# Performance work log

Hardware: AMD Instinct MI355X
Metric: run time of the kernel (lower is better)

## Reference

```python
import jax, jax.numpy as jnp
import numpy as np
import math

VOCAB = 32000
D = 1024
SEQ = 2048
BATCH = 4
PAD_IDX = 0
LN_EPS = 1e-5


def make_sinusoidal_pe(max_len, d):
    position = jnp.arange(max_len, dtype=jnp.float32)[:, None]
    div_term = jnp.exp(jnp.arange(0, d, 2, dtype=jnp.float32) * (-math.log(10000.0) / d))
    ang = position * div_term  # [max_len, d/2]
    pe = jnp.zeros((max_len, d), dtype=jnp.float32)
    pe = pe.at[:, 0::2].set(jnp.sin(ang))
    pe = pe.at[:, 1::2].set(jnp.cos(ang))
    return pe


def verse_weights(verse_positions):
    # weight = 1.2 at the first token of each nonzero-verse run (zeros are skipped
    # and do not reset the run), else 1.0. Vectorized via forward-fill of the
    # last nonzero verse id strictly before each position.
    v = verse_positions  # [B, S] int
    S = v.shape[1]
    idx = jnp.where(v != 0, jnp.arange(S)[None, :], -1)
    last_idx = jax.lax.cummax(idx, axis=1)
    prev_idx = jnp.concatenate([jnp.full_like(last_idx[:, :1], -1), last_idx[:, :-1]], axis=1)
    prev_verse = jnp.take_along_axis(v, jnp.clip(prev_idx, 0, None), axis=1)
    prev_verse = jnp.where(prev_idx >= 0, prev_verse, -1)
    return jnp.where((v != 0) & (v != prev_verse), 1.2, 1.0).astype(jnp.float32)


def setup_inputs() -> dict:
    key = jax.random.key(0)
    k1, k2, k3, k4, k5, k6, k7 = jax.random.split(key, 7)
    token_ids = jax.random.randint(k1, (BATCH, SEQ), 0, VOCAB)
    verse_positions = jnp.sort(jax.random.randint(k2, (BATCH, SEQ), 0, 200), axis=-1)
    book_types = jax.random.randint(k3, (BATCH, SEQ), 0, 4)
    # Xavier-uniform embedding table with padding row zeroed
    limit = math.sqrt(6.0 / (VOCAB + D))
    emb_table = jax.random.uniform(k4, (VOCAB, D), jnp.float32, -limit, limit)
    emb_table = emb_table.at[PAD_IDX].set(0.0)
    book_table = jax.random.normal(k5, (4, D), jnp.float32)
    ln_gamma = jnp.ones((D,), jnp.float32)
    ln_beta = jnp.zeros((D,), jnp.float32)
    return {
        "token_ids": token_ids,
        "verse_positions": verse_positions,
        "book_types": book_types,
        "emb_table": emb_table,
        "book_table": book_table,
        "ln_gamma": ln_gamma,
        "ln_beta": ln_beta,
    }


def reference(token_ids, verse_positions, book_types, emb_table, book_table, ln_gamma, ln_beta):
    # Token embedding * sqrt(d)
    x = emb_table[token_ids] * jnp.asarray(math.sqrt(D), jnp.float32)  # [B,S,D]
    # Verse-weighted sinusoidal positional encoding (dropout = identity, eval mode)
    pe = make_sinusoidal_pe(SEQ, D)[None, :, :]  # [1,S,D]
    w = verse_weights(verse_positions)  # [B,S]
    x = x + pe * w[:, :, None]
    # Book-type embedding
    x = x + book_table[book_types]
    # LayerNorm
    mu = jnp.mean(x, axis=-1, keepdims=True)
    var = jnp.mean(jnp.square(x - mu), axis=-1, keepdims=True)
    x = (x - mu) * jax.lax.rsqrt(var + LN_EPS) * ln_gamma + ln_beta
    return x
```

## Files before the change

kernel.cpp:

```cpp
#include <hip/hip_runtime.h>

#define VOCAB 32000
#define DIM   1024
#define SEQ_  2048
#define NBAT  4

__global__ __launch_bounds__(256) void verse_embed_ln_kernel(
    const int*   __restrict__ token_ids,
    const int*   __restrict__ verse_pos,
    const int*   __restrict__ book_types,
    const float* __restrict__ emb_table,
    const float* __restrict__ book_table,
    const float* __restrict__ gamma,
    const float* __restrict__ beta,
    float*       __restrict__ out)
{
    const int wid  = threadIdx.x >> 6;
    const int lane = threadIdx.x & 63;
    const int row  = (blockIdx.x << 2) + wid;
    const int s    = row & (SEQ_ - 1);

    const int tok   = token_ids[row];
    const int bt    = book_types[row];
    const int v     = verse_pos[row];
    const int vprev = (s == 0) ? -1 : verse_pos[row - 1];
    const float w = (v != 0 && v != vprev) ? 1.2f : 1.0f;

    const float* __restrict__ erow = emb_table  + (size_t)tok * DIM;
    const float* __restrict__ brow = book_table + (size_t)bt  * DIM;

    float4 e[4], bk[4];
    #pragma unroll
    for (int c = 0; c < 4; ++c) {
        const int d0 = (c << 8) + (lane << 2);
        e[c]  = *reinterpret_cast<const float4*>(erow + d0);
        bk[c] = *reinterpret_cast<const float4*>(brow + d0);
    }

    const float C2  = -13.287712379549449f / 1024.0f;
    const float sf  = (float)s;
    const float SQD = 32.0f;

    float x[16];
    float sum = 0.0f, sq = 0.0f;
    #pragma unroll
    for (int c = 0; c < 4; ++c) {
        const int d0 = (c << 8) + (lane << 2);
        const float f0 = exp2f(C2 * (float)d0);
        const float f1 = exp2f(C2 * (float)(d0 + 2));
        float s0, c0, s1, c1;
        __sincosf(sf * f0, &s0, &c0);
        __sincosf(sf * f1, &s1, &c1);
        const float x0 = e[c].x * SQD + s0 * w + bk[c].x;
        const float x1 = e[c].y * SQD + c0 * w + bk[c].y;
        const float x2 = e[c].z * SQD + s1 * w + bk[c].z;
        const float x3 = e[c].w * SQD + c1 * w + bk[c].w;
        x[4 * c + 0] = x0; x[4 * c + 1] = x1; x[4 * c + 2] = x2; x[4 * c + 3] = x3;
        sum += (x0 + x1) + (x2 + x3);
        sq  += (x0 * x0 + x1 * x1) + (x2 * x2 + x3 * x3);
    }

    #pragma unroll
    for (int off = 32; off >= 1; off >>= 1) {
        sum += __shfl_xor(sum, off, 64);
        sq  += __shfl_xor(sq,  off, 64);
    }

    const float mean = sum * (1.0f / (float)DIM);
    const float var  = sq * (1.0f / (float)DIM) - mean * mean;
    const float rstd = rsqrtf(var + 1e-5f);

    float* __restrict__ orow = out + (size_t)row * DIM;
    #pragma unroll
    for (int c = 0; c < 4; ++c) {
        const int d0 = (c << 8) + (lane << 2);
        const float4 g  = *reinterpret_cast<const float4*>(gamma + d0);
        const float4 bb = *reinterpret_cast<const float4*>(beta  + d0);
        float4 o;
        o.x = (x[4 * c + 0] - mean) * rstd * g.x + bb.x;
        o.y = (x[4 * c + 1] - mean) * rstd * g.y + bb.y;
        o.z = (x[4 * c + 2] - mean) * rstd * g.z + bb.z;
        o.w = (x[4 * c + 3] - mean) * rstd * g.w + bb.w;
        *reinterpret_cast<float4*>(orow + d0) = o;
    }
}

extern "C" void kernel_launch(void* const* d_in, const int* in_sizes, int n_in,
                              void* d_out, int out_size, void* d_ws, size_t ws_size,
                              hipStream_t stream) {
    const int*   token_ids  = (const int*)d_in[0];
    const int*   verse_pos  = (const int*)d_in[1];
    const int*   book_types = (const int*)d_in[2];
    const float* emb_table  = (const float*)d_in[3];
    const float* book_table = (const float*)d_in[4];
    const float* ln_gamma   = (const float*)d_in[5];
    const float* ln_beta    = (const float*)d_in[6];
    float* out = (float*)d_out;

    dim3 grid((NBAT * SEQ_) / 4);
    dim3 block(256);
    verse_embed_ln_kernel<<<grid, block, 0, stream>>>(
        token_ids, verse_pos, book_types, emb_table, book_table,
        ln_gamma, ln_beta, out);
}
```

Before: 16.51 us.

## Process two rows per wave, stage book table in LDS, reuse frequency terms

Each wavefront now handles two consecutive rows, and the grid is halved. The 4-row book table is staged into shared memory once per block, and gamma/beta are loaded once per wave and reused for both rows. Per-element exp2 frequency computation is replaced by one exp2 per lane, with later frequencies derived by multiplying with constants. This cuts redundant global loads and transcendental work. In exchange it adds a block-wide sync, higher register pressure, and fewer blocks.

Result: no change. 16.49 us (-0.1%).

```diff
diff --git a/kernel.cpp b/kernel.cpp
--- a/kernel.cpp
+++ b/kernel.cpp
@@ -1,6 +1,5 @@
 #include <hip/hip_runtime.h>
 
-#define VOCAB 32000
 #define DIM   1024
 #define SEQ_  2048
 #define NBAT  4
@@ -15,73 +14,94 @@
     const float* __restrict__ beta,
     float*       __restrict__ out)
 {
-    const int wid  = threadIdx.x >> 6;
-    const int lane = threadIdx.x & 63;
-    const int row  = (blockIdx.x << 2) + wid;
-    const int s    = row & (SEQ_ - 1);
+    __shared__ float4 bookLDS[1024];
 
-    const int tok   = token_ids[row];
-    const int bt    = book_types[row];
-    const int v     = verse_pos[row];
-    const int vprev = (s == 0) ? -1 : verse_pos[row - 1];
-    const float w = (v != 0 && v != vprev) ? 1.2f : 1.0f;
+    const int t    = threadIdx.x;
+    const int wid  = t >> 6;
+    const int lane = t & 63;
+    const int base = ((blockIdx.x << 2) + wid) << 1;
 
-    const float* __restrict__ erow = emb_table  + (size_t)tok * DIM;
-    const float* __restrict__ brow = book_table + (size_t)bt  * DIM;
+    const float4* __restrict__ bt4 = reinterpret_cast<const float4*>(book_table);
+    #pragma unroll
+    for (int k = 0; k < 4; ++k)
+        bookLDS[k * 256 + t] = bt4[k * 256 + t];
 
-    float4 e[4], bk[4];
+    const int tok0 = token_ids[base],   tok1 = token_ids[base + 1];
+    const int bt0  = book_types[base],  bt1  = book_types[base + 1];
+    const int v0   = verse_pos[base],   v1   = verse_pos[base + 1];
+    const int s0   = base & (SEQ_ - 1);
+    const int vp0  = (s0 == 0) ? -1 : verse_pos[base - 1];
+    const float w0 = (v0 != 0 && v0 != vp0) ? 1.2f : 1.0f;
+    const float w1 = (v1 != 0 && v1 != v0)  ? 1.2f : 1.0f;
+
+    const float4* __restrict__ er0 = reinterpret_cast<const float4*>(emb_table) + (size_t)tok0 * 256;
+    const float4* __restrict__ er1 = reinterpret_cast<const float4*>(emb_table) + (size_t)tok1 * 256;
+    float4 e[2][4];
     #pragma unroll
-    for (int c = 0; c < 4; ++c) {
-        const int d0 = (c << 8) + (lane << 2);
-        e[c]  = *reinterpret_cast<const float4*>(erow + d0);
-        bk[c] = *reinterpret_cast<const float4*>(brow + d0);
-    }
+    for (int c = 0; c < 4; ++c) e[0][c] = er0[c * 64 + lane];
+    #pragma unroll
+    for (int c = 0; c < 4; ++c) e[1][c] = er1[c * 64 + lane];
 
-    const float C2  = -13.287712379549449f / 1024.0f;
-    const float sf  = (float)s;
+    const float4* __restrict__ g4 = reinterpret_cast<const float4*>(gamma);
+    const float4* __restrict__ b4 = reinterpret_cast<const float4*>(beta);
+    float4 g[4], b[4];
+    #pragma unroll
+    for (int c = 0; c < 4; ++c) { g[c] = g4[c * 64 + lane]; b[c] = b4[c * 64 + lane]; }
+
+    const float C2 = -13.287712379549449f / 1024.0f;
+    const float K2 = 0.9821718931198913f;
+    const int   dl = lane << 2;
+    const float fb0 = exp2f(C2 * (float)dl);
     const float SQD = 32.0f;
 
-    float x[16];
-    float sum = 0.0f, sq = 0.0f;
-    #pragma unroll
-    for (int c = 0; c < 4; ++c) {
-        const int d0 = (c << 8) + (lane << 2);
-        const float f0 = exp2f(C2 * (float)d0);
-        const float f1 = exp2f(C2 * (float)(d0 + 2));
-        float s0, c0, s1, c1;
-        __sincosf(sf * f0, &s0, &c0);
-        __sincosf(sf * f1, &s1, &c1);
-        const float x0 = e[c].x * SQD + s0 * w + bk[c].x;
-        const float x1 = e[c].y * SQD + c0 * w + bk[c].y;
-        const float x2 = e[c].z * SQD + s1 * w + bk[c].z;
-        const float x3 = e[c].w * SQD + c1 * w + bk[c].w;
-        x[4 * c + 0] = x0; x[4 * c + 1] = x1; x[4 * c + 2] = x2; x[4 * c + 3] = x3;
-        sum += (x0 + x1) + (x2 + x3);
-        sq  += (x0 * x0 + x1 * x1) + (x2 * x2 + x3 * x3);
-    }
+    __syncthreads();
 
     #pragma unroll
-    for (int off = 32; off >= 1; off >>= 1) {
-        sum += __shfl_xor(sum, off, 64);
-        sq  += __shfl_xor(sq,  off, 64);
-    }
+    for (int r = 0; r < 2; ++r) {
+        const int row = base + r;
+        const float sf = (float)(row & (SEQ_ - 1));
+        const float w  = r ? w1 : w0;
+        const int  bt  = r ? bt1 : bt0;
+        const float4* __restrict__ bkl = &bookLDS[bt * 256];
 
-    const float mean = sum * (1.0f / (float)DIM);
-    const float var  = sq * (1.0f / (float)DIM) - mean * mean;
-    const float rstd = rsqrtf(var + 1e-5f);
+        float4 x[4];
+        float sum = 0.0f, sq = 0.0f;
+        float fb = fb0;
+        #pragma unroll
+        for (int c = 0; c < 4; ++c) {
+            const float a0 = sf * fb;
+            const float a1 = sf * (fb * K2);
+            const float sn0 = __sinf(a0), cs0 = __cosf(a0);
+            const float sn1 = __sinf(a1), cs1 = __cosf(a1);
+            fb *= 0.1f;
+            const float4 bk = bkl[c * 64 + lane];
+            x[c].x = e[r][c].x * SQD + sn0 * w + bk.x;
+            x[c].y = e[r][c].y * SQD + cs0 * w + bk.y;
+            x[c].z = e[r][c].z * SQD + sn1 * w + bk.z;
+            x[c].w = e[r][c].w * SQD + cs1 * w + bk.w;
+            sum += (x[c].x + x[c].y) + (x[c].z + x[c].w);
+            sq  += (x[c].x * x[c].x + x[c].y * x[c].y) + (x[c].z * x[c].z + x[c].w * x[c].w);
+        }
 
-    float* __restrict__ orow = out + (size_t)row * DIM;
-    #pragma unroll
-    for (int c = 0; c < 4; ++c) {
-        const int d0 = (c << 8) + (lane << 2);
-        const float4 g  = *reinterpret_cast<const float4*>(gamma + d0);
-        const float4 bb = *reinterpret_cast<const float4*>(beta  + d0);
-        float4 o;
-        o.x = (x[4 * c + 0] - mean) * rstd * g.x + bb.x;
-        o.y = (x[4 * c + 1] - mean) * rstd * g.y + bb.y;
-        o.z = (x[4 * c + 2] - mean) * rstd * g.z + bb.z;
-        o.w = (x[4 * c + 3] - mean) * rstd * g.w + bb.w;
-        *reinterpret_cast<float4*>(orow + d0) = o;
+        #pragma unroll
+        for (int off = 32; off >= 1; off >>= 1) {
+            sum += __shfl_xor(sum, off, 64);
+            sq  += __shfl_xor(sq,  off, 64);
+        }
+        const float mean = sum * (1.0f / (float)DIM);
+        const float var  = sq * (1.0f / (float)DIM) - mean * mean;
+        const float rstd = rsqrtf(var + 1e-5f);
+
+        float4* __restrict__ orow = reinterpret_cast<float4*>(out) + (size_t)row * 256;
+        #pragma unroll
+        for (int c = 0; c < 4; ++c) {
+            float4 o;
+            o.x = (x[c].x - mean) * rstd * g[c].x + b[c].x;
+            o.y = (x[c].y - mean) * rstd * g[c].y + b[c].y;
+            o.z = (x[c].z - mean) * rstd * g[c].z + b[c].z;
+            o.w = (x[c].w - mean) * rstd * g[c].w + b[c].w;
+            orow[c * 64 + lane] = o;
+        }
     }
 }
 
@@ -97,7 +117,7 @@
     const float* ln_beta    = (const float*)d_in[6];
     float* out = (float*)d_out;
 
-    dim3 grid((NBAT * SEQ_) / 4);
+    dim3 grid((NBAT * SEQ_) / 8);
     dim3 block(256);
     verse_embed_ln_kernel<<<grid, block, 0, stream>>>(
         token_ids, verse_pos, book_types, emb_table, book_table,
```
